# Kernel optimization log

Measured on AMD Instinct MI355X. Metric: run time of the kernel, lower is better.

Reference implementation:

```python
import jax, jax.numpy as jnp
import numpy as np

B, T, K, H = 8, 1024, 512, 8


def setup_inputs() -> dict:
    key = jax.random.key(0)
    kx, kq, kk, kv, ko = jax.random.split(key, 5)
    s = 0.02
    return {
        "x": jax.random.normal(kx, (B, T, K), dtype=jnp.float32),
        "Wq": jax.random.normal(kq, (K * H, K), dtype=jnp.float32) * s,
        "Wk": jax.random.normal(kk, (K * H, K), dtype=jnp.float32) * s,
        "Wv": jax.random.normal(kv, (K * H, K), dtype=jnp.float32) * s,
        "Wo": jax.random.normal(ko, (K, K * H), dtype=jnp.float32) * s,
    }


def reference(x, Wq, Wk, Wv, Wo):
    b, t, k = x.shape
    h = H
    scale = k ** 0.25  # applied to both q and k, total 1/sqrt(k)
    # torch Linear: y = x @ W.T ; view (b,t,h,k) then move heads out: (b,h,t,k)
    def proj(W):
        return (x @ W.T).reshape(b, t, h, k).transpose(0, 2, 1, 3)
    q = proj(Wq) / scale
    kk_ = proj(Wk) / scale
    v = proj(Wv)
    dot = jnp.einsum("bhtd,bhsd->bhts", q, kk_)  # (b,h,t,t)
    # causal mask: strict upper triangle (j > i) -> -inf
    causal = jnp.tril(jnp.ones((t, t), dtype=bool))
    dot = jnp.where(causal[None, None], dot, -jnp.inf)
    attn = jax.nn.softmax(dot, axis=-1)
    out = jnp.einsum("bhts,bhsd->bhtd", attn, v)  # (b,h,t,k)
    out = out.transpose(0, 2, 1, 3).reshape(b, t, h * k)
    return out @ Wo.T
```

## Files before the change

kernel.cpp:

```cpp
#include <hip/hip_runtime.h>
#include <hip/hip_bf16.h>
#include <cstdint>
#include <cmath>


typedef __attribute__((ext_vector_type(8))) short short8;
typedef __attribute__((ext_vector_type(4))) float f32x4;

#define DEVINL __device__ __forceinline__

DEVINL float bf2f(ushort u) { union { uint32_t i; float f; } w; w.i = (uint32_t)u << 16; return w.f; }
DEVINL ushort f2bf(float f) {
  union { float f; uint32_t i; } w; w.f = f;
  uint32_t r = w.i + 0x7FFFu + ((w.i >> 16) & 1u);
  return (ushort)(r >> 16);
}

DEVINL void gl_lds16(const ushort* g, ushort* l) {
  __builtin_amdgcn_global_load_lds(
      (const __attribute__((address_space(1))) uint32_t*)g,
      (__attribute__((address_space(3))) uint32_t*)l, 16, 0, 0);
}

DEVINL int csw(int row, int col) {
  return row * 128 + ((((col >> 4) ^ ((row >> 2) & 7)) << 4) | (col & 15));
}

__global__ __launch_bounds__(256) void cvt_f32_bf16(const float* __restrict__ in,
                                                    ushort* __restrict__ out,
                                                    int n8, float scale) {
  int i = blockIdx.x * 256 + threadIdx.x;
  if (i >= n8) return;
  const float4* p = (const float4*)in + (size_t)i * 2;
  float4 a = p[0], b = p[1];
  short8 o;
  o[0] = (short)f2bf(a.x * scale); o[1] = (short)f2bf(a.y * scale);
  o[2] = (short)f2bf(a.z * scale); o[3] = (short)f2bf(a.w * scale);
  o[4] = (short)f2bf(b.x * scale); o[5] = (short)f2bf(b.y * scale);
  o[6] = (short)f2bf(b.z * scale); o[7] = (short)f2bf(b.w * scale);
  ((short8*)out)[i] = o;
}

__global__ __launch_bounds__(256) void zerof4(float4* __restrict__ p, int n4) {
  int i = blockIdx.x * 256 + threadIdx.x;
  if (i < n4) p[i] = float4{0.f, 0.f, 0.f, 0.f};
}

template<bool CSKIP, bool CKB, int EPI, bool ZBH>
__global__ __launch_bounds__(256) void gemm_bt(
    const ushort* __restrict__ A0, long long sAb, long long sAh,
    const ushort* __restrict__ B0, long long sBb, long long sBh,
    void* __restrict__ C0, long long sCb, long long sCh,
    int lda, int ldb, int ldc, int K)
{
  const int bm = blockIdx.x, bn = blockIdx.y, bz = blockIdx.z;
  if (CSKIP && bn > bm) return;
  long long za, zb, zc;
  if (ZBH) {
    const long long bi = bz >> 3, hi = bz & 7;
    za = bi * sAb + hi * sAh; zb = bi * sBb + hi * sBh; zc = bi * sCb + hi * sCh;
  } else {
    za = (long long)bz * sAh; zb = (long long)bz * sBh; zc = (long long)bz * sCh;
  }
  const ushort* A = A0 + za;
  const ushort* B = B0 + zb;
  int kend = K;
  if (CKB) { int kb = (bm + 1) * 128; kend = kb < K ? kb : K; }

  __shared__ ushort smem[16384];

  const int tid = threadIdx.x;
  const int wave = tid >> 6, lane = tid & 63;
  const int wr = wave >> 1, wc = wave & 1;
  const int l15 = lane & 15, kq = lane >> 4;

  const ushort* ag = A + (size_t)(bm * 128 + wave * 16 + (lane >> 2)) * lda + (lane & 3) * 8;
  const ushort* bg = B + (size_t)(bn * 128 + wave * 16 + (lane >> 2)) * ldb + (lane & 3) * 8;
  const size_t aoff = (size_t)64 * lda, boff = (size_t)64 * ldb;

  auto STAGE = [&](int buf, int kk) {
    ushort* al = &smem[buf * 8192 + wave * 16 * 32];
    ushort* bl = al + 4096;
    gl_lds16(ag + kk, al);
    gl_lds16(ag + kk + aoff, al + 64 * 32);
    gl_lds16(bg + kk, bl);
    gl_lds16(bg + kk + boff, bl + 64 * 32);
  };

  f32x4 acc[4][4] = {};
  const int nt = kend >> 5;

  STAGE(0, 0);
  for (int t = 0; t < nt; ++t) {
    const int cur = t & 1;
    if (t + 1 < nt) {
      STAGE(cur ^ 1, (t + 1) << 5);
      asm volatile("s_waitcnt vmcnt(4)" ::: "memory");
    } else {
      asm volatile("s_waitcnt vmcnt(0)" ::: "memory");
    }
    __builtin_amdgcn_s_barrier();
    __builtin_amdgcn_sched_barrier(0);

    const ushort* As = &smem[cur * 8192];
    const ushort* Bs = As + 4096;
    short8 af[4], bfr[4];
#pragma unroll
    for (int m = 0; m < 4; ++m)
      af[m] = *(const short8*)&As[(wr * 64 + m * 16 + l15) * 32 + kq * 8];
#pragma unroll
    for (int n = 0; n < 4; ++n)
      bfr[n] = *(const short8*)&Bs[(wc * 64 + n * 16 + l15) * 32 + kq * 8];
#pragma unroll
    for (int m = 0; m < 4; ++m)
#pragma unroll
      for (int n = 0; n < 4; ++n)
        acc[m][n] = __builtin_amdgcn_mfma_f32_16x16x32_bf16(af[m], bfr[n], acc[m][n], 0, 0, 0);

    __builtin_amdgcn_s_barrier();
    __builtin_amdgcn_sched_barrier(0);
  }

  if constexpr (EPI == 0) {
    ushort* C = (ushort*)C0 + zc;
#pragma unroll
    for (int m = 0; m < 4; ++m)
#pragma unroll
      for (int n = 0; n < 4; ++n)
#pragma unroll
        for (int r = 0; r < 4; ++r)
          smem[csw(wr * 64 + m * 16 + kq * 4 + r, wc * 64 + n * 16 + l15)] = f2bf(acc[m][n][r]);
    __syncthreads();
    const int col = (tid & 15) * 8;
#pragma unroll
    for (int j = 0; j < 8; ++j) {
      const int rr = j * 16 + (tid >> 4);
      *(short8*)&C[(size_t)(bm * 128 + rr) * ldc + bn * 128 + col] =
          *(const short8*)&smem[csw(rr, col)];
    }
  } else {
    float* C = (float*)C0 + zc;
    const int r0 = bm * 128 + wr * 64 + (lane >> 4) * 4;
    const int c0 = bn * 128 + wc * 64 + l15;
#pragma unroll
    for (int m = 0; m < 4; ++m)
#pragma unroll
      for (int n = 0; n < 4; ++n)
#pragma unroll
        for (int r = 0; r < 4; ++r)
          atomicAdd(&C[(size_t)(r0 + m * 16 + r) * ldc + (c0 + n * 16)], acc[m][n][r]);
  }
}

__global__ __launch_bounds__(256) void transposeV(const ushort* __restrict__ QKVg,
                                                  ushort* __restrict__ Vtg) {
  __shared__ ushort tile[64][72];
  const int bx = blockIdx.x;
  const int by = blockIdx.y;
  const int bz = blockIdx.z;
  const int b = bz >> 3, h = bz & 7;
  const int t = threadIdx.x;
  const int r = t >> 2, c = (t & 3) * 16;

  const ushort* src = QKVg + (size_t)(b * 1024 + bx * 64 + r) * 12288 + 8192 + h * 512 + by * 64 + c;
  short8 v0 = *(const short8*)src;
  short8 v1 = *(const short8*)(src + 8);
#pragma unroll
  for (int j = 0; j < 8; ++j) { tile[r][c + j] = (ushort)v0[j]; tile[r][c + 8 + j] = (ushort)v1[j]; }
  __syncthreads();

  ushort* dst = Vtg + (size_t)(bz * 512 + by * 64 + r) * 1024 + bx * 64 + c;
  short8 o0, o1;
#pragma unroll
  for (int j = 0; j < 8; ++j) { o0[j] = (short)tile[c + j][r]; o1[j] = (short)tile[c + 8 + j][r]; }
  *(short8*)dst = o0;
  *(short8*)(dst + 8) = o1;
}

__global__ __launch_bounds__(256) void softmax_causal(ushort* __restrict__ S) {
  const int wave = threadIdx.x >> 6, lane = threadIdx.x & 63;
  const size_t row_id = (size_t)blockIdx.x * 4 + wave;
  const int t = (int)(row_id & 1023);
  ushort* row = S + row_id * 1024;
  const int j0 = lane * 16;

  short8 v0 = *(const short8*)&row[j0];
  short8 v1 = *(const short8*)&row[j0 + 8];
  float f[16];
#pragma unroll
  for (int i = 0; i < 8; ++i) { f[i] = bf2f((ushort)v0[i]); f[8 + i] = bf2f((ushort)v1[i]); }

  float m = -1e30f;
#pragma unroll
  for (int i = 0; i < 16; ++i) {
    if (j0 + i > t) f[i] = -1e30f;
    m = fmaxf(m, f[i]);
  }
#pragma unroll
  for (int off = 32; off; off >>= 1) m = fmaxf(m, __shfl_xor(m, off));

  float s = 0.f;
#pragma unroll
  for (int i = 0; i < 16; ++i) { f[i] = __expf(f[i] - m); s += f[i]; }
#pragma unroll
  for (int off = 32; off; off >>= 1) s += __shfl_xor(s, off);
  const float inv = 1.f / s;

#pragma unroll
  for (int i = 0; i < 8; ++i) {
    v0[i] = (short)f2bf(f[i] * inv);
    v1[i] = (short)f2bf(f[8 + i] * inv);
  }
  *(short8*)&row[j0] = v0;
  *(short8*)&row[j0 + 8] = v1;
}

extern "C" void kernel_launch(void* const* d_in, const int* in_sizes, int n_in,
                              void* d_out, int out_size, void* d_ws, size_t ws_size,
                              hipStream_t stream) {
  const float* x  = (const float*)d_in[0];
  const float* Wq = (const float*)d_in[1];
  const float* Wk = (const float*)d_in[2];
  const float* Wv = (const float*)d_in[3];
  const float* Wo = (const float*)d_in[4];
  float* out = (float*)d_out;

  const int g = (ws_size >= 293601280ull) ? 4 : (ws_size >= 192937984ull) ? 2 : 1;
  const int ng = 8 / g;

  ushort* xb   = (ushort*)d_ws;
  ushort* Wqkv = xb   + (size_t)4194304;
  ushort* Wob  = Wqkv + (size_t)6291456;
  ushort* AO   = Wob  + (size_t)2097152;
  ushort* QKVg = AO   + (size_t)33554432;
  ushort* Vtg  = QKVg + (size_t)g * 12582912;
  ushort* Sg   = Vtg  + (size_t)g * 4194304;

  const float iscale = (float)(1.0 / pow(512.0, 0.25));

  cvt_f32_bf16<<<2048, 256, 0, stream>>>(x,  xb,             524288, 1.0f);
  cvt_f32_bf16<<<1024, 256, 0, stream>>>(Wq, Wqkv,           262144, iscale);
  cvt_f32_bf16<<<1024, 256, 0, stream>>>(Wk, Wqkv + 2097152, 262144, iscale);
  cvt_f32_bf16<<<1024, 256, 0, stream>>>(Wv, Wqkv + 4194304, 262144, 1.0f);
  cvt_f32_bf16<<<1024, 256, 0, stream>>>(Wo, Wob,            262144, 1.0f);

  for (int grp = 0; grp < ng; ++grp) {
    gemm_bt<false, false, 0, false><<<dim3(g * 8, 96, 1), 256, 0, stream>>>(
        xb + (size_t)grp * g * 524288, 0, 0,
        Wqkv, 0, 0,
        QKVg, 0, 0,
        512, 512, 12288, 512);

    transposeV<<<dim3(16, 8, 8 * g), 256, 0, stream>>>(QKVg, Vtg);

    gemm_bt<true, false, 0, true><<<dim3(8, 8, 8 * g), 256, 0, stream>>>(
        QKVg,        12582912LL, 512LL,
        QKVg + 4096, 12582912LL, 512LL,
        Sg,          8388608LL,  1048576LL,
        12288, 12288, 1024, 512);

    softmax_causal<<<g * 2048, 256, 0, stream>>>(Sg);

    gemm_bt<false, true, 0, true><<<dim3(8, 4, 8 * g), 256, 0, stream>>>(
        Sg,  8388608LL, 1048576LL,
        Vtg, 4194304LL, 524288LL,
        AO + (size_t)grp * g * 4194304, 4194304LL, 512LL,
        1024, 1024, 4096, 1024);
  }

  zerof4<<<4096, 256, 0, stream>>>((float4*)out, 1048576);
  gemm_bt<false, false, 2, false><<<dim3(64, 4, 4), 256, 0, stream>>>(
      AO,  0, 1024LL,
      Wob, 0, 1024LL,
      out, 0, 0LL,
      4096, 4096, 512, 1024);
}
```

Baseline: 556.8 us.

## Add 256x256-tile 512-thread bf16 MFMA GEMM for QKV, QK^T and PV

Adds a new GEMM kernel with 256x256 output tiles, 8 waves per block, double-buffered LDS staging through global_load_lds, and an LDS-swizzled bf16 epilogue. It replaces the three per-group GEMMs (QKV projection, scores, attention·V) that previously used the smaller-tile gemm_bt. The goal is more data reuse per tile and fewer global loads. The trade-offs are 128 KB of LDS per block, fewer blocks (lower occupancy and poorer causal-skip granularity, since whole 256-wide tiles are skipped or computed), and heavy register use.

```diff
diff --git a/kernel.cpp b/kernel.cpp
--- a/kernel.cpp
+++ b/kernel.cpp
@@ -44,6 +44,116 @@
 __global__ __launch_bounds__(256) void zerof4(float4* __restrict__ p, int n4) {
   int i = blockIdx.x * 256 + threadIdx.x;
   if (i < n4) p[i] = float4{0.f, 0.f, 0.f, 0.f};
+}
+
+template<bool CSKIP, bool CKB, bool ZBH>
+__global__ __launch_bounds__(512, 2) void gemm256(
+    const ushort* __restrict__ A0, long long sAb, long long sAh,
+    const ushort* __restrict__ B0, long long sBb, long long sBh,
+    ushort* __restrict__ C0, long long sCb, long long sCh,
+    int lda, int ldb, int ldc, int K)
+{
+  const int bm = blockIdx.x, bn = blockIdx.y, bz = blockIdx.z;
+  if (CSKIP && bn > bm) return;
+  long long za, zb, zc;
+  if (ZBH) {
+    const long long bi = bz >> 3, hi = bz & 7;
+    za = bi * sAb + hi * sAh; zb = bi * sBb + hi * sBh; zc = bi * sCb + hi * sCh;
+  } else {
+    za = (long long)bz * sAh; zb = (long long)bz * sBh; zc = (long long)bz * sCh;
+  }
+  const ushort* A = A0 + za;
+  const ushort* B = B0 + zb;
+  int kend = K;
+  if (CKB) { int kb = (bm + 1) * 256; kend = kb < K ? kb : K; }
+
+  __shared__ ushort smem[65536];
+
+  const int tid = threadIdx.x;
+  const int wid = tid >> 6, lane = tid & 63;
+  const int wr = wid >> 2, wc = wid & 3;
+  const int l15 = lane & 15, kq = lane >> 4;
+
+  const int srow = wid * 8 + (lane >> 3);
+  const int scol = ((lane & 7) ^ ((lane >> 3) & 7)) * 8;
+  const ushort* agbase = A + (size_t)(bm * 256 + srow) * lda + scol;
+  const ushort* bgbase = B + (size_t)(bn * 256 + srow) * ldb + scol;
+
+  auto STAGE = [&](int buf, int kk) {
+    ushort* a = &smem[buf * 32768 + wid * 512];
+    ushort* b = a + 16384;
+#pragma unroll
+    for (int q = 0; q < 4; ++q) {
+      gl_lds16(agbase + (size_t)q * 64 * lda + kk, a + q * 4096);
+      gl_lds16(bgbase + (size_t)q * 64 * ldb + kk, b + q * 4096);
+    }
+  };
+
+  f32x4 acc[8][4] = {};
+  const int nt = kend >> 6;
+
+  STAGE(0, 0);
+  for (int t = 0; t < nt; ++t) {
+    const int cur = t & 1;
+    if (t + 1 < nt) {
+      STAGE(cur ^ 1, (t + 1) << 6);
+      asm volatile("s_waitcnt vmcnt(8)" ::: "memory");
+    } else {
+      asm volatile("s_waitcnt vmcnt(0)" ::: "memory");
+    }
+    __builtin_amdgcn_sched_barrier(0);
+    __builtin_amdgcn_s_barrier();
+    __builtin_amdgcn_sched_barrier(0);
+
+    const ushort* As = &smem[cur * 32768];
+    const ushort* Bs = As + 16384;
+    short8 bfr[4][2];
+#pragma unroll
+    for (int n = 0; n < 4; ++n)
+#pragma unroll
+      for (int ks = 0; ks < 2; ++ks)
+        bfr[n][ks] = *(const short8*)
+            &Bs[(wc * 64 + n * 16 + l15) * 64 + (((ks * 4 + kq) ^ (l15 & 7)) * 8)];
+#pragma unroll
+    for (int m = 0; m < 8; ++m) {
+      short8 a0 = *(const short8*)
+          &As[(wr * 128 + m * 16 + l15) * 64 + (((0 + kq) ^ (l15 & 7)) * 8)];
+      short8 a1 = *(const short8*)
+          &As[(wr * 128 + m * 16 + l15) * 64 + (((4 + kq) ^ (l15 & 7)) * 8)];
+      __builtin_amdgcn_s_setprio(1);
+#pragma unroll
+      for (int n = 0; n < 4; ++n) {
+        acc[m][n] = __builtin_amdgcn_mfma_f32_16x16x32_bf16(a0, bfr[n][0], acc[m][n], 0, 0, 0);
+        acc[m][n] = __builtin_amdgcn_mfma_f32_16x16x32_bf16(a1, bfr[n][1], acc[m][n], 0, 0, 0);
+      }
+      __builtin_amdgcn_s_setprio(0);
+    }
+    __builtin_amdgcn_sched_barrier(0);
+    asm volatile("s_waitcnt lgkmcnt(0)" ::: "memory");
+    __builtin_amdgcn_sched_barrier(0);
+    __builtin_amdgcn_s_barrier();
+    __builtin_amdgcn_sched_barrier(0);
+  }
+
+#pragma unroll
+  for (int m = 0; m < 8; ++m)
+#pragma unroll
+    for (int n = 0; n < 4; ++n)
+#pragma unroll
+      for (int r = 0; r < 4; ++r) {
+        const int row = wr * 128 + m * 16 + kq * 4 + r;
+        const int col = wc * 64 + n * 16 + l15;
+        smem[row * 256 + (((col >> 3) ^ (row & 31)) * 8) + (col & 7)] = f2bf(acc[m][n][r]);
+      }
+  __syncthreads();
+  ushort* C = C0 + zc;
+#pragma unroll
+  for (int j = 0; j < 16; ++j) {
+    const int chi = j * 512 + tid;
+    const int row = chi >> 5, cc = chi & 31;
+    *(short8*)&C[(size_t)(bm * 256 + row) * ldc + bn * 256 + cc * 8] =
+        *(const short8*)&smem[row * 256 + ((cc ^ (row & 31)) * 8)];
+  }
 }
 
 template<bool CSKIP, bool CKB, int EPI, bool ZBH>
@@ -245,7 +355,7 @@
   cvt_f32_bf16<<<1024, 256, 0, stream>>>(Wo, Wob,            262144, 1.0f);
 
   for (int grp = 0; grp < ng; ++grp) {
-    gemm_bt<false, false, 0, false><<<dim3(g * 8, 96, 1), 256, 0, stream>>>(
+    gemm256<false, false, false><<<dim3(g * 4, 48, 1), 512, 0, stream>>>(
         xb + (size_t)grp * g * 524288, 0, 0,
         Wqkv, 0, 0,
         QKVg, 0, 0,
@@ -253,7 +363,7 @@
 
     transposeV<<<dim3(16, 8, 8 * g), 256, 0, stream>>>(QKVg, Vtg);
 
-    gemm_bt<true, false, 0, true><<<dim3(8, 8, 8 * g), 256, 0, stream>>>(
+    gemm256<true, false, true><<<dim3(4, 4, 8 * g), 512, 0, stream>>>(
         QKVg,        12582912LL, 512LL,
         QKVg + 4096, 12582912LL, 512LL,
         Sg,          8388608LL,  1048576LL,
@@ -261,7 +371,7 @@
 
     softmax_causal<<<g * 2048, 256, 0, stream>>>(Sg);
 
-    gemm_bt<false, true, 0, true><<<dim3(8, 4, 8 * g), 256, 0, stream>>>(
+    gemm256<false, true, true><<<dim3(4, 2, 8 * g), 512, 0, stream>>>(
         Sg,  8388608LL, 1048576LL,
         Vtg, 4194304LL, 524288LL,
         AO + (size_t)grp * g * 4194304, 4194304LL, 512LL,
```

After: 597.7 us. +7.4%, slower.

## Replace 128x128 GEMM with 256x256 tile, 512-thread, BK=64 pipelined kernel

Applied to the files above, without the earlier changes.

Swaps the 128x128x32 bf16 MFMA GEMM for a 256x256x64 tile run by 8 waves (512 threads). Global-to-LDS loads are split into four phases that interleave with the MFMA sub-steps. LDS uses an XOR swizzle to avoid bank conflicts, and s_setprio is raised around the MFMA blocks. The larger tiles give more data reuse per load and fewer barriers, at the cost of 128KB of LDS per block, fewer blocks per launch (lower occupancy and worse wave quantization), and coarser causal skipping in the QK^T and PV GEMMs.

```diff
diff --git a/kernel.cpp b/kernel.cpp
--- a/kernel.cpp
+++ b/kernel.cpp
@@ -20,10 +20,6 @@
   __builtin_amdgcn_global_load_lds(
       (const __attribute__((address_space(1))) uint32_t*)g,
       (__attribute__((address_space(3))) uint32_t*)l, 16, 0, 0);
-}
-
-DEVINL int csw(int row, int col) {
-  return row * 128 + ((((col >> 4) ^ ((row >> 2) & 7)) << 4) | (col & 15));
 }
 
 __global__ __launch_bounds__(256) void cvt_f32_bf16(const float* __restrict__ in,
@@ -47,7 +43,7 @@
 }
 
 template<bool CSKIP, bool CKB, int EPI, bool ZBH>
-__global__ __launch_bounds__(256) void gemm_bt(
+__global__ __launch_bounds__(512, 2) void gemm256(
     const ushort* __restrict__ A0, long long sAb, long long sAh,
     const ushort* __restrict__ B0, long long sBb, long long sBh,
     void* __restrict__ C0, long long sCb, long long sCh,
@@ -65,90 +61,127 @@
   const ushort* A = A0 + za;
   const ushort* B = B0 + zb;
   int kend = K;
-  if (CKB) { int kb = (bm + 1) * 128; kend = kb < K ? kb : K; }
-
-  __shared__ ushort smem[16384];
+  if (CKB) { int kb = (bm + 1) * 256; kend = kb < K ? kb : K; }
+
+  __shared__ ushort smem[65536];
 
   const int tid = threadIdx.x;
-  const int wave = tid >> 6, lane = tid & 63;
-  const int wr = wave >> 1, wc = wave & 1;
+  const int wid = tid >> 6, lane = tid & 63;
+  const int wr = wid >> 2, wc = wid & 3;
   const int l15 = lane & 15, kq = lane >> 4;
 
-  const ushort* ag = A + (size_t)(bm * 128 + wave * 16 + (lane >> 2)) * lda + (lane & 3) * 8;
-  const ushort* bg = B + (size_t)(bn * 128 + wave * 16 + (lane >> 2)) * ldb + (lane & 3) * 8;
-  const size_t aoff = (size_t)64 * lda, boff = (size_t)64 * ldb;
-
-  auto STAGE = [&](int buf, int kk) {
-    ushort* al = &smem[buf * 8192 + wave * 16 * 32];
-    ushort* bl = al + 4096;
-    gl_lds16(ag + kk, al);
-    gl_lds16(ag + kk + aoff, al + 64 * 32);
-    gl_lds16(bg + kk, bl);
-    gl_lds16(bg + kk + boff, bl + 64 * 32);
+  const int srow8 = lane >> 3;
+  const int schunk = ((lane & 7) ^ srow8) * 8;
+  const ushort* ag = A + (size_t)(bm * 256 + wid * 8 + srow8) * lda + schunk;
+  const ushort* bg = B + (size_t)(bn * 256 + wid * 8 + srow8) * ldb + schunk;
+
+  auto STA = [&](int buf, int band, int kk) {
+    gl_lds16(ag + (size_t)band * 64 * lda + kk, &smem[buf * 32768 + band * 4096 + wid * 512]);
   };
-
-  f32x4 acc[4][4] = {};
-  const int nt = kend >> 5;
-
-  STAGE(0, 0);
+  auto STB = [&](int buf, int band, int kk) {
+    gl_lds16(bg + (size_t)band * 64 * ldb + kk, &smem[buf * 32768 + 16384 + band * 4096 + wid * 512]);
+  };
+  auto STAGE2 = [&](int buf, int p, int kk) {
+    switch (p) {
+      case 0: STB(buf, 0, kk); STB(buf, 1, kk); break;
+      case 1: STB(buf, 2, kk); STB(buf, 3, kk); break;
+      case 2: STA(buf, 0, kk); STA(buf, 2, kk); break;
+      default: STA(buf, 1, kk); STA(buf, 3, kk); break;
+    }
+  };
+
+  f32x4 acc[8][4] = {};
+  const int nt = kend >> 6;
+
+#pragma unroll
+  for (int p = 0; p < 4; ++p) STAGE2(0, p, 0);
+
+  short8 bq[4];
   for (int t = 0; t < nt; ++t) {
     const int cur = t & 1;
-    if (t + 1 < nt) {
-      STAGE(cur ^ 1, (t + 1) << 5);
-      asm volatile("s_waitcnt vmcnt(4)" ::: "memory");
-    } else {
-      asm volatile("s_waitcnt vmcnt(0)" ::: "memory");
+    const ushort* As = &smem[cur * 32768];
+    const ushort* Bs = As + 16384;
+    const bool pre = (t + 1 < nt);
+    const int kk1 = (t + 1) << 6;
+
+#pragma unroll
+    for (int ph = 0; ph < 4; ++ph) {
+      const int mh = ph & 1, ks = ph >> 1;
+      if (pre) STAGE2(cur ^ 1, ph, kk1);
+      if (ph == 0) {
+        if (pre) asm volatile("s_waitcnt vmcnt(4)" ::: "memory");
+        else     asm volatile("s_waitcnt vmcnt(2)" ::: "memory");
+        __builtin_amdgcn_sched_barrier(0);
+        __builtin_amdgcn_s_barrier();
+        __builtin_amdgcn_sched_barrier(0);
+      } else if (ph == 1) {
+        if (pre) asm volatile("s_waitcnt vmcnt(4)" ::: "memory");
+        else     asm volatile("s_waitcnt vmcnt(0)" ::: "memory");
+        __builtin_amdgcn_sched_barrier(0);
+        __builtin_amdgcn_s_barrier();
+        __builtin_amdgcn_sched_barrier(0);
+      }
+
+      if (mh == 0) {
+#pragma unroll
+        for (int n = 0; n < 4; ++n)
+          bq[n] = *(const short8*)
+              &Bs[(wc * 64 + n * 16 + l15) * 64 + (((ks * 4 + kq) ^ (l15 & 7)) * 8)];
+      }
+      short8 av[4];
+#pragma unroll
+      for (int m = 0; m < 4; ++m)
+        av[m] = *(const short8*)
+            &As[(wr * 128 + mh * 64 + m * 16 + l15) * 64 + (((ks * 4 + kq) ^ (l15 & 7)) * 8)];
+
+      __builtin_amdgcn_s_setprio(1);
+#pragma unroll
+      for (int m = 0; m < 4; ++m)
+#pragma unroll
+        for (int n = 0; n < 4; ++n)
+          acc[mh * 4 + m][n] =
+              __builtin_amdgcn_mfma_f32_16x16x32_bf16(av[m], bq[n], acc[mh * 4 + m][n], 0, 0, 0);
+      __builtin_amdgcn_s_setprio(0);
+
+      if (ph == 3) {
+        asm volatile("s_waitcnt lgkmcnt(0)" ::: "memory");
+        __builtin_amdgcn_sched_barrier(0);
+        __builtin_amdgcn_s_barrier();
+        __builtin_amdgcn_sched_barrier(0);
+      }
     }
-    __builtin_amdgcn_s_barrier();
-    __builtin_amdgcn_sched_barrier(0);
-
-    const ushort* As = &smem[cur * 8192];
-    const ushort* Bs = As + 4096;
-    short8 af[4], bfr[4];
-#pragma unroll
-    for (int m = 0; m < 4; ++m)
-      af[m] = *(const short8*)&As[(wr * 64 + m * 16 + l15) * 32 + kq * 8];
-#pragma unroll
-    for (int n = 0; n < 4; ++n)
-      bfr[n] = *(const short8*)&Bs[(wc * 64 + n * 16 + l15) * 32 + kq * 8];
-#pragma unroll
-    for (int m = 0; m < 4; ++m)
+  }
+
+  if constexpr (EPI == 0) {
+#pragma unroll
+    for (int m = 0; m < 8; ++m)
 #pragma unroll
       for (int n = 0; n < 4; ++n)
-        acc[m][n] = __builtin_amdgcn_mfma_f32_16x16x32_bf16(af[m], bfr[n], acc[m][n], 0, 0, 0);
-
-    __builtin_amdgcn_s_barrier();
-    __builtin_amdgcn_sched_barrier(0);
-  }
-
-  if constexpr (EPI == 0) {
+#pragma unroll
+        for (int r = 0; r < 4; ++r) {
+          const int row = wr * 128 + m * 16 + kq * 4 + r;
+          const int col = wc * 64 + n * 16 + l15;
+          smem[row * 256 + (((col >> 3) ^ (row & 31)) * 8) + (col & 7)] = f2bf(acc[m][n][r]);
+        }
+    __syncthreads();
     ushort* C = (ushort*)C0 + zc;
 #pragma unroll
-    for (int m = 0; m < 4; ++m)
-#pragma unroll
-      for (int n = 0; n < 4; ++n)
-#pragma unroll
-        for (int r = 0; r < 4; ++r)
-          smem[csw(wr * 64 + m * 16 + kq * 4 + r, wc * 64 + n * 16 + l15)] = f2bf(acc[m][n][r]);
-    __syncthreads();
-    const int col = (tid & 15) * 8;
-#pragma unroll
-    for (int j = 0; j < 8; ++j) {
-      const int rr = j * 16 + (tid >> 4);
-      *(short8*)&C[(size_t)(bm * 128 + rr) * ldc + bn * 128 + col] =
-          *(const short8*)&smem[csw(rr, col)];
+    for (int j = 0; j < 16; ++j) {
+      const int chi = j * 512 + tid;
+      const int row = chi >> 5, cc = chi & 31;
+      *(short8*)&C[(size_t)(bm * 256 + row) * ldc + bn * 256 + cc * 8] =
+          *(const short8*)&smem[row * 256 + ((cc ^ (row & 31)) * 8)];
     }
   } else {
     float* C = (float*)C0 + zc;
-    const int r0 = bm * 128 + wr * 64 + (lane >> 4) * 4;
-    const int c0 = bn * 128 + wc * 64 + l15;
-#pragma unroll
-    for (int m = 0; m < 4; ++m)
+#pragma unroll
+    for (int m = 0; m < 8; ++m)
 #pragma unroll
       for (int n = 0; n < 4; ++n)
 #pragma unroll
         for (int r = 0; r < 4; ++r)
-          atomicAdd(&C[(size_t)(r0 + m * 16 + r) * ldc + (c0 + n * 16)], acc[m][n][r]);
+          atomicAdd(&C[(size_t)(bm * 256 + wr * 128 + m * 16 + kq * 4 + r) * ldc
+                       + bn * 256 + wc * 64 + n * 16 + l15], acc[m][n][r]);
   }
 }
 
@@ -245,7 +278,7 @@
   cvt_f32_bf16<<<1024, 256, 0, stream>>>(Wo, Wob,            262144, 1.0f);
 
   for (int grp = 0; grp < ng; ++grp) {
-    gemm_bt<false, false, 0, false><<<dim3(g * 8, 96, 1), 256, 0, stream>>>(
+    gemm256<false, false, 0, false><<<dim3(g * 4, 48, 1), 512, 0, stream>>>(
         xb + (size_t)grp * g * 524288, 0, 0,
         Wqkv, 0, 0,
         QKVg, 0, 0,
@@ -253,7 +286,7 @@
 
     transposeV<<<dim3(16, 8, 8 * g), 256, 0, stream>>>(QKVg, Vtg);
 
-    gemm_bt<true, false, 0, true><<<dim3(8, 8, 8 * g), 256, 0, stream>>>(
+    gemm256<true, false, 0, true><<<dim3(4, 4, 8 * g), 512, 0, stream>>>(
         QKVg,        12582912LL, 512LL,
         QKVg + 4096, 12582912LL, 512LL,
         Sg,          8388608LL,  1048576LL,
@@ -261,7 +294,7 @@
 
     softmax_causal<<<g * 2048, 256, 0, stream>>>(Sg);
 
-    gemm_bt<false, true, 0, true><<<dim3(8, 4, 8 * g), 256, 0, stream>>>(
+    gemm256<false, true, 0, true><<<dim3(4, 2, 8 * g), 512, 0, stream>>>(
         Sg,  8388608LL, 1048576LL,
         Vtg, 4194304LL, 524288LL,
         AO + (size_t)grp * g * 4194304, 4194304LL, 512LL,
@@ -269,7 +302,7 @@
   }
 
   zerof4<<<4096, 256, 0, stream>>>((float4*)out, 1048576);
-  gemm_bt<false, false, 2, false><<<dim3(64, 4, 4), 256, 0, stream>>>(
+  gemm256<false, false, 2, false><<<dim3(32, 2, 4), 512, 0, stream>>>(
       AO,  0, 1024LL,
       Wob, 0, 1024LL,
       out, 0, 0LL,
```

Measured after the change: 558.7 us. About the same (+0.4%).
